# Kernel optimization log

Measured on AMD Instinct MI355X. Metric: run time of the kernel, lower is better.

The kernel has to match this reference:

```python
import jax, jax.numpy as jnp
import numpy as np


def squash(s):
    # s: (..., d); v = ||s|| / (1 + ||s||^2) * s
    norm = jnp.linalg.norm(s, axis=-1, keepdims=True)
    return norm / (1.0 + norm * norm) * s


def setup_inputs() -> dict:
    key = jax.random.key(0)
    k1, k2, k3 = jax.random.split(key, 3)
    batch, n_in, d_in, n_out, d_out = 256, 1152, 8, 10, 16
    u_i = jax.random.normal(k1, (batch, n_in, d_in), dtype=jnp.float32)
    weight = jax.random.normal(k2, (1, n_in, n_out, d_in, d_out), dtype=jnp.float32)
    bias = jax.random.normal(k3, (n_in, n_out, 1), dtype=jnp.float32)
    return {"u_i": u_i, "weight": weight, "bias": bias, "r": 3}


def reference(u_i, weight, bias, r):
    batch, n_in, d_in = u_i.shape
    # predictions u_j|i: (batch, n_in, n_out, d_out)
    u_ji = jnp.einsum('bnd,node->bnoe', u_i, weight[0]) + bias  # bias (n_in,n_out,1) broadcasts over d_out
    # dynamic routing
    b = jnp.zeros(u_ji.shape[:3], dtype=u_ji.dtype)  # (batch, n_in, n_out)
    v = None
    for _ in range(r):  # r is a small static iteration count
        c = jax.nn.softmax(b, axis=-1)                      # over n_out
        s = jnp.einsum('bno,bnoe->boe', c, u_ji)            # weighted sum over n_in
        v = squash(s)                                       # (batch, n_out, d_out)
        b = b + jnp.einsum('bnoe,boe->bno', u_ji, v)        # agreement update
    return v
```

## Files before the change

### kernel.cpp

```cpp
#include <hip/hip_runtime.h>


#define B    256
#define N    1152
#define NO   10
#define DI   8
#define DE   16
#define NTILE   8
#define NTILES  144
#define BG      64
#define BGS     4
#define THREADS 320

#define SP_OFF 0
#define SP_SZ  (NTILES * B * NO * DE)
#define VS_OFF (SP_OFF + SP_SZ)
#define VS_SZ  (B * NO * DE)

__global__ __launch_bounds__(THREADS, 3)
void routing_kernel(const float* __restrict__ u,
                    const float* __restrict__ w,
                    const float* __restrict__ bias,
                    const float* __restrict__ vsum,
                    float* __restrict__ s_part,
                    const int has_v) {
    __shared__ float lgx[NO][BG];
    const int tid  = threadIdx.x;
    const int lane = tid & 63;
    const int wv   = __builtin_amdgcn_readfirstlane(tid >> 6);
    const int o0   = wv * 2;
    const int b    = blockIdx.y * BG + lane;
    const int n0   = blockIdx.x * NTILE;

    float4 vv[2][4];
#pragma unroll
    for (int oi = 0; oi < 2; ++oi)
#pragma unroll
        for (int eq = 0; eq < 4; ++eq)
            vv[oi][eq] = make_float4(0.f, 0.f, 0.f, 0.f);
    if (has_v) {
#pragma unroll
        for (int oi = 0; oi < 2; ++oi)
#pragma unroll
            for (int eq = 0; eq < 4; ++eq)
                vv[oi][eq] = *(const float4*)(vsum + ((size_t)b * NO + o0 + oi) * DE + eq * 4);
    }

    float4 acc[2][4];
#pragma unroll
    for (int oi = 0; oi < 2; ++oi)
#pragma unroll
        for (int eq = 0; eq < 4; ++eq)
            acc[oi][eq] = make_float4(0.f, 0.f, 0.f, 0.f);

    for (int i = 0; i < NTILE; ++i) {
        const int n = n0 + i;

        const float* up = u + ((size_t)b * N + n) * DI;
        const float4 u0 = *(const float4*)up;
        const float4 u1 = *(const float4*)(up + 4);
        const float ur[DI] = {u0.x, u0.y, u0.z, u0.w, u1.x, u1.y, u1.z, u1.w};

        const float* wp = w + ((size_t)n * NO + o0) * (DI * DE);
        float4 uji[2][4];
#pragma unroll
        for (int oi = 0; oi < 2; ++oi) {
            const float bv = bias[n * NO + o0 + oi];
#pragma unroll
            for (int eq = 0; eq < 4; ++eq)
                uji[oi][eq] = make_float4(bv, bv, bv, bv);
#pragma unroll
            for (int d = 0; d < DI; ++d) {
                const float* wrow = wp + oi * (DI * DE) + d * DE;
#pragma unroll
                for (int eq = 0; eq < 4; ++eq) {
                    const float4 w4 = *(const float4*)(wrow + eq * 4);
                    uji[oi][eq].x += ur[d] * w4.x;
                    uji[oi][eq].y += ur[d] * w4.y;
                    uji[oi][eq].z += ur[d] * w4.z;
                    uji[oi][eq].w += ur[d] * w4.w;
                }
            }
        }

        float c[2];
        if (has_v) {
#pragma unroll
            for (int oi = 0; oi < 2; ++oi) {
                float lg = 0.f;
#pragma unroll
                for (int eq = 0; eq < 4; ++eq)
                    lg += uji[oi][eq].x * vv[oi][eq].x + uji[oi][eq].y * vv[oi][eq].y
                        + uji[oi][eq].z * vv[oi][eq].z + uji[oi][eq].w * vv[oi][eq].w;
                lgx[o0 + oi][lane] = lg;
            }
            __syncthreads();
            float l[NO];
#pragma unroll
            for (int o = 0; o < NO; ++o) l[o] = lgx[o][lane];
            __syncthreads();

            float m = l[0];
#pragma unroll
            for (int o = 1; o < NO; ++o) m = fmaxf(m, l[o]);
            float sum = 0.f;
#pragma unroll
            for (int o = 0; o < NO; ++o) { l[o] = __expf(l[o] - m); sum += l[o]; }
            const float inv = 1.f / sum;
            c[0] = l[o0] * inv;
            c[1] = l[o0 + 1] * inv;
        } else {
            c[0] = 0.1f; c[1] = 0.1f;
        }

#pragma unroll
        for (int oi = 0; oi < 2; ++oi)
#pragma unroll
            for (int eq = 0; eq < 4; ++eq) {
                acc[oi][eq].x += c[oi] * uji[oi][eq].x;
                acc[oi][eq].y += c[oi] * uji[oi][eq].y;
                acc[oi][eq].z += c[oi] * uji[oi][eq].z;
                acc[oi][eq].w += c[oi] * uji[oi][eq].w;
            }
    }

    float* sp = s_part + (((size_t)blockIdx.x * B + b) * NO + o0) * DE;
#pragma unroll
    for (int oi = 0; oi < 2; ++oi)
#pragma unroll
        for (int eq = 0; eq < 4; ++eq)
            *(float4*)(sp + oi * DE + eq * 4) = acc[oi][eq];
}

__global__ __launch_bounds__(256)
void squash_kernel(const float* __restrict__ s_part,
                   float* __restrict__ vsum,
                   float* __restrict__ out,
                   const int accum) {
    const int t0 = blockIdx.x * 256 + threadIdx.x;
    const int q  = t0 & 3;
    const int g  = t0 >> 2;

    float s = 0.f;
    const float* sp = s_part + (size_t)(q * 36) * (B * NO * DE) + g;
#pragma unroll 9
    for (int i = 0; i < 36; ++i)
        s += sp[(size_t)i * (B * NO * DE)];
    s += __shfl_xor(s, 1);
    s += __shfl_xor(s, 2);

    float nsq = s * s;
#pragma unroll
    for (int msk = 4; msk <= 32; msk <<= 1) nsq += __shfl_xor(nsq, msk);
    const float nrm   = sqrtf(nsq);
    const float scale = nrm / (1.f + nsq);
    const float val   = s * scale;

    if (q == 0) {
        out[g]  = val;
        vsum[g] = accum ? (vsum[g] + val) : val;
    }
}

extern "C" void kernel_launch(void* const* d_in, const int* in_sizes, int n_in,
                              void* d_out, int out_size, void* d_ws, size_t ws_size,
                              hipStream_t stream) {
    const float* u    = (const float*)d_in[0];
    const float* w    = (const float*)d_in[1];
    const float* bias = (const float*)d_in[2];

    float* wsf    = (float*)d_ws;
    float* s_part = wsf + SP_OFF;
    float* vsum   = wsf + VS_OFF;
    float* out    = (float*)d_out;

    for (int it = 0; it < 3; ++it) {
        routing_kernel<<<dim3(NTILES, BGS), THREADS, 0, stream>>>(
            u, w, bias, vsum, s_part, it > 0);
        squash_kernel<<<(4 * B * NO * DE) / 256, 256, 0, stream>>>(
            s_part, vsum, out, it > 0);
    }
}
```

Before: 195.1 us.

## Pre-transpose u for coalesced loads and double-buffer logits to drop a barrier

Adds a transpose kernel that repacks u into a [n][half][b][4] layout, so lanes reading consecutive batch indices hit contiguous float4s in the routing kernel instead of loads strided by N*DI. The layout is used only when the workspace is large enough. The shared logit buffer is also double-buffered by iteration parity, which removes the second __syncthreads per n step. The cost is an extra kernel launch, extra workspace traffic, and reliance on the workspace size check.

New measurement: 205.5 us. 5.3% more time.

```diff
diff --git a/kernel.cpp b/kernel.cpp
--- a/kernel.cpp
+++ b/kernel.cpp
@@ -16,15 +16,32 @@
 #define SP_SZ  (NTILES * B * NO * DE)
 #define VS_OFF (SP_OFF + SP_SZ)
 #define VS_SZ  (B * NO * DE)
+#define UT_OFF (VS_OFF + VS_SZ)
+#define UT_SZ  (2 * N * B * 4)
+
+__global__ __launch_bounds__(256)
+void transpose_kernel(const float* __restrict__ u, float* __restrict__ ut) {
+    const int lane = threadIdx.x & 63;
+    const int wv   = threadIdx.x >> 6;
+    const int n    = blockIdx.x * 4 + wv;
+    const int b    = blockIdx.y * 64 + lane;
+    const float* up = u + ((size_t)b * N + n) * DI;
+    const float4 a0 = *(const float4*)up;
+    const float4 a1 = *(const float4*)(up + 4);
+    *(float4*)(ut + ((size_t)(n * 2 + 0) * B + b) * 4) = a0;
+    *(float4*)(ut + ((size_t)(n * 2 + 1) * B + b) * 4) = a1;
+}
 
 __global__ __launch_bounds__(THREADS, 3)
 void routing_kernel(const float* __restrict__ u,
+                    const float* __restrict__ ut,
                     const float* __restrict__ w,
                     const float* __restrict__ bias,
                     const float* __restrict__ vsum,
                     float* __restrict__ s_part,
-                    const int has_v) {
-    __shared__ float lgx[NO][BG];
+                    const int has_v,
+                    const int use_ut) {
+    __shared__ float lgx[2][NO][BG];
     const int tid  = threadIdx.x;
     const int lane = tid & 63;
     const int wv   = __builtin_amdgcn_readfirstlane(tid >> 6);
@@ -56,9 +73,16 @@
     for (int i = 0; i < NTILE; ++i) {
         const int n = n0 + i;
 
-        const float* up = u + ((size_t)b * N + n) * DI;
-        const float4 u0 = *(const float4*)up;
-        const float4 u1 = *(const float4*)(up + 4);
+        float4 u0, u1;
+        if (use_ut) {
+            const float* up = ut + ((size_t)(n * 2) * B + b) * 4;
+            u0 = *(const float4*)up;
+            u1 = *(const float4*)(up + B * 4);
+        } else {
+            const float* up = u + ((size_t)b * N + n) * DI;
+            u0 = *(const float4*)up;
+            u1 = *(const float4*)(up + 4);
+        }
         const float ur[DI] = {u0.x, u0.y, u0.z, u0.w, u1.x, u1.y, u1.z, u1.w};
 
         const float* wp = w + ((size_t)n * NO + o0) * (DI * DE);
@@ -85,6 +109,7 @@
 
         float c[2];
         if (has_v) {
+            const int pb = i & 1;
 #pragma unroll
             for (int oi = 0; oi < 2; ++oi) {
                 float lg = 0.f;
@@ -92,13 +117,12 @@
                 for (int eq = 0; eq < 4; ++eq)
                     lg += uji[oi][eq].x * vv[oi][eq].x + uji[oi][eq].y * vv[oi][eq].y
                         + uji[oi][eq].z * vv[oi][eq].z + uji[oi][eq].w * vv[oi][eq].w;
-                lgx[o0 + oi][lane] = lg;
+                lgx[pb][o0 + oi][lane] = lg;
             }
             __syncthreads();
             float l[NO];
 #pragma unroll
-            for (int o = 0; o < NO; ++o) l[o] = lgx[o][lane];
-            __syncthreads();
+            for (int o = 0; o < NO; ++o) l[o] = lgx[pb][o][lane];
 
             float m = l[0];
 #pragma unroll
@@ -172,11 +196,17 @@
     float* wsf    = (float*)d_ws;
     float* s_part = wsf + SP_OFF;
     float* vsum   = wsf + VS_OFF;
+    float* ut     = wsf + UT_OFF;
     float* out    = (float*)d_out;
+
+    const int use_ut = (ws_size >= (size_t)(SP_SZ + VS_SZ + UT_SZ) * sizeof(float));
+
+    if (use_ut)
+        transpose_kernel<<<dim3(N / 4, B / 64), 256, 0, stream>>>(u, ut);
 
     for (int it = 0; it < 3; ++it) {
         routing_kernel<<<dim3(NTILES, BGS), THREADS, 0, stream>>>(
-            u, w, bias, vsum, s_part, it > 0);
+            u, ut, w, bias, vsum, s_part, it > 0, use_ut);
         squash_kernel<<<(4 * B * NO * DE) / 256, 256, 0, stream>>>(
             s_part, vsum, out, it > 0);
     }
```
